# Kernel tuning notes

Measured on AMD Instinct MI355X. Metric: run time of the kernel, lower is better.

Reference implementation:

```python
import jax, jax.numpy as jnp
import numpy as np
import math

IN_DIM = 256
OUT_DIM = 256
MAX_IN = 1024
MAX_OUT = 512
BATCH = 2
SEQ = 1024  # actual_seq_len == max_in_seq here
RED = 2
LN_EPS = 1e-5


def setup_inputs() -> dict:
    key = jax.random.key(0)
    ks = jax.random.split(key, 8)
    N = BATCH * SEQ
    return {
        "x": jax.random.normal(ks[0], (N, IN_DIM), dtype=jnp.float32),
        "M": jax.random.uniform(ks[1], (OUT_DIM, IN_DIM), minval=-0.5, maxval=0.5, dtype=jnp.float32),
        "P": jax.random.uniform(ks[2], (OUT_DIM, OUT_DIM), minval=-0.1, maxval=0.1, dtype=jnp.float32),
        "Linker": jax.random.uniform(ks[3], (MAX_IN, MAX_OUT), minval=-0.1, maxval=0.1, dtype=jnp.float32),
        "ln_gamma": jnp.ones((OUT_DIM,), dtype=jnp.float32),
        "ln_beta": jnp.zeros((OUT_DIM,), dtype=jnp.float32),
        "res_W": jax.random.uniform(ks[4], (OUT_DIM, IN_DIM), minval=-0.1, maxval=0.1, dtype=jnp.float32),
        "res_linker": jax.random.uniform(ks[5], (MAX_IN, MAX_OUT), minval=-0.1, maxval=0.1, dtype=jnp.float32),
        "actual_seq_len": SEQ,
    }


def _layer_norm(z, gamma, beta):
    mu = jnp.mean(z, axis=-1, keepdims=True)
    var = jnp.mean((z - mu) ** 2, axis=-1, keepdims=True)
    return (z - mu) * jax.lax.rsqrt(var + LN_EPS) * gamma + beta


def _periods():
    i = jnp.arange(OUT_DIM, dtype=jnp.float32)[:, None]
    j = jnp.arange(OUT_DIM, dtype=jnp.float32)[None, :]
    return i * OUT_DIM + j + 2.0  # (D, D)


def reference(x, M, P, Linker, ln_gamma, ln_beta, res_W, res_linker, actual_seq_len):
    S = int(actual_seq_len)
    N, _ = x.shape
    B = N // S
    D = OUT_DIM
    out_seq = max(1, S // RED)

    # Z = LN(x @ M^T)
    Z = _layer_norm(x @ M.T, ln_gamma, ln_beta)  # (N, D)

    # position transform: T[k,i] = sum_j Z[k,j] * P[i,j] * cos(2*pi*k / periods[i,j])
    k = jnp.arange(N, dtype=jnp.float32)[:, None, None]  # (N,1,1)
    phi = jnp.cos(2.0 * math.pi * k / _periods()[None])   # (N, D, D)
    T = jnp.einsum('kj,ij,kij->ki', Z, P, phi)            # (N, D)

    # adaptive sequence-length transform via Linker slice
    L = Linker[:S, :out_seq]                               # (S, out_seq)
    U = jnp.einsum('bsd,st->btd', T.reshape(B, S, D), L).reshape(B * out_seq, D)

    # 'separate' residual path
    rfeat = (x @ res_W.T).reshape(B, S, D)
    rL = res_linker[:S, :out_seq]
    residual = jnp.einsum('bsd,st->btd', rfeat, rL).reshape(B * out_seq, D)

    return U + residual
```

## Files before the change

kernel.cpp:

```cpp
#include <hip/hip_runtime.h>

#define D256 256
#define KT 8
#define S_SEQ 1024
#define OUTSEQ 512

typedef __attribute__((ext_vector_type(8))) short bf16x8;
typedef __attribute__((ext_vector_type(8))) unsigned short u16x8;
typedef __attribute__((ext_vector_type(4))) float f32x4;

__device__ inline unsigned short f2bf(float f) {
  unsigned u = __float_as_uint(f);
  return (unsigned short)((u + 0x7fffu + ((u >> 16) & 1u)) >> 16);
}

__global__ __launch_bounds__(256) void k_prep(const float* __restrict__ M,
                                              const float* __restrict__ resW,
                                              const float* __restrict__ P,
                                              const float* __restrict__ Linker,
                                              const float* __restrict__ rLinker,
                                              float2* __restrict__ MW,
                                              float4* __restrict__ PIt4,
                                              unsigned short* __restrict__ LinkTb) {
  __shared__ float tl[64][65];
  const int tid = threadIdx.x;
  if (blockIdx.x < 256) {
    const int j = blockIdx.x;
    const int t = tid;
    MW[j * D256 + t] = make_float2(M[t * D256 + j], resW[t * D256 + j]);
    const float p = (float)(t * D256 + j + 2);
    const float ip = 1.0f / p;
    const float cb2 = 2.0f * __builtin_amdgcn_cosf(ip);
    PIt4[j * D256 + t] = make_float4(P[t * D256 + j], ip, cb2, 0.0f);
    return;
  }
  const int tb = blockIdx.x - 256;
  const int st = tb & 31;
  const int tt = tb >> 5;
  const int s0 = st * 64, t0 = tt * 64;
  const float* src = (s0 < 1024) ? (Linker + (size_t)s0 * OUTSEQ)
                                 : (rLinker + (size_t)(s0 - 1024) * OUTSEQ);
  {
    const int sy = tid >> 2, sx = tid & 3;
    #pragma unroll
    for (int c = 0; c < 4; ++c) {
      const int ci = sx + c * 4;
      const float4 v = *(const float4*)&src[sy * OUTSEQ + t0 + ci * 4];
      tl[ci * 4 + 0][sy] = v.x;
      tl[ci * 4 + 1][sy] = v.y;
      tl[ci * 4 + 2][sy] = v.z;
      tl[ci * 4 + 3][sy] = v.w;
    }
  }
  __syncthreads();
  {
    const int ty = tid >> 2, tx = tid & 3;
    u16x8 o0, o1;
    #pragma unroll
    for (int e = 0; e < 8; ++e) o0[e] = f2bf(tl[ty][tx * 16 + e]);
    #pragma unroll
    for (int e = 0; e < 8; ++e) o1[e] = f2bf(tl[ty][tx * 16 + 8 + e]);
    unsigned short* dst = LinkTb + (size_t)(t0 + ty) * 2048 + s0 + tx * 16;
    *(u16x8*)dst = o0;
    *(u16x8*)(dst + 8) = o1;
  }
}

__global__ __launch_bounds__(1024, 4) void k_AB(const float* __restrict__ x,
                                                const float2* __restrict__ MW,
                                                const float4* __restrict__ PIt4,
                                                const float* __restrict__ gamma,
                                                const float* __restrict__ beta,
                                                unsigned short* __restrict__ Bt) {
  __shared__ float Xs[D256][12];
  __shared__ float red[4][KT][D256];
  __shared__ float mu_s[KT], rs_s[KT];
  const int tid = threadIdx.x;
  const int i = tid & 255;
  const int h = tid >> 8;
  const int j0 = h * 64;
  const int k0 = blockIdx.x * KT;

  Xs[i][h]     = x[(k0 + h) * D256 + i];
  Xs[i][h + 4] = x[(k0 + h + 4) * D256 + i];
  __syncthreads();

  float aM[KT], aR[KT];
  #pragma unroll
  for (int r = 0; r < KT; ++r) { aM[r] = 0.f; aR[r] = 0.f; }
  {
    const float2* mwp = MW + i;
    #pragma unroll 8
    for (int jj = 0; jj < 64; ++jj) {
      const int j = j0 + jj;
      const float2 mw = mwp[j * D256];
      const float4 z0 = *(const float4*)&Xs[j][0];
      const float4 z1 = *(const float4*)&Xs[j][4];
      aM[0] = fmaf(z0.x, mw.x, aM[0]); aR[0] = fmaf(z0.x, mw.y, aR[0]);
      aM[1] = fmaf(z0.y, mw.x, aM[1]); aR[1] = fmaf(z0.y, mw.y, aR[1]);
      aM[2] = fmaf(z0.z, mw.x, aM[2]); aR[2] = fmaf(z0.z, mw.y, aR[2]);
      aM[3] = fmaf(z0.w, mw.x, aM[3]); aR[3] = fmaf(z0.w, mw.y, aR[3]);
      aM[4] = fmaf(z1.x, mw.x, aM[4]); aR[4] = fmaf(z1.x, mw.y, aR[4]);
      aM[5] = fmaf(z1.y, mw.x, aM[5]); aR[5] = fmaf(z1.y, mw.y, aR[5]);
      aM[6] = fmaf(z1.z, mw.x, aM[6]); aR[6] = fmaf(z1.z, mw.y, aR[6]);
      aM[7] = fmaf(z1.w, mw.x, aM[7]); aR[7] = fmaf(z1.w, mw.y, aR[7]);
    }
  }

  #pragma unroll
  for (int r = 0; r < KT; ++r) red[h][r][i] = aR[r];
  __syncthreads();
  if (tid < 256) {
    u16x8 o;
    #pragma unroll
    for (int r = 0; r < KT; ++r)
      o[r] = f2bf(red[0][r][tid] + red[1][r][tid] + red[2][r][tid] + red[3][r][tid]);
    *(u16x8*)(Bt + (size_t)tid * 4096 + 2048 + k0) = o;
  }
  __syncthreads();

  #pragma unroll
  for (int r = 0; r < KT; ++r) red[h][r][i] = aM[r];
  __syncthreads();
  #pragma unroll
  for (int p = 0; p < 2; ++p) {
    const int r = h * 2 + p;
    Xs[i][r] = red[0][r][i] + red[1][r][i] + red[2][r][i] + red[3][r][i];
  }
  __syncthreads();

  const int w = tid >> 6, lane = tid & 63;
  if (w < KT) {
    float s = 0.f, sq = 0.f;
    #pragma unroll
    for (int l = 0; l < 4; ++l) {
      const float v = Xs[lane + 64 * l][w];
      s += v;
      sq = fmaf(v, v, sq);
    }
    #pragma unroll
    for (int off = 32; off; off >>= 1) {
      s += __shfl_down(s, off);
      sq += __shfl_down(sq, off);
    }
    if (lane == 0) {
      const float m = s * (1.0f / 256.0f);
      const float var = sq * (1.0f / 256.0f) - m * m;
      mu_s[w] = m;
      rs_s[w] = rsqrtf(var + 1e-5f);
    }
  }
  __syncthreads();
  {
    const float g = gamma[i], be = beta[i];
    #pragma unroll
    for (int p = 0; p < 2; ++p) {
      const int r = h + 4 * p;
      Xs[i][r] = (Xs[i][r] - mu_s[r]) * rs_s[r] * g + be;
    }
  }
  __syncthreads();

  float accT[KT] = {};
  const float kf0 = (float)k0, kf1 = (float)(k0 + 1);
  {
    const float4* pip = PIt4 + i;
    #pragma unroll 4
    for (int jj = 0; jj < 64; ++jj) {
      const int j = j0 + jj;
      const float4 pi = pip[j * D256];
      const float4 z0 = *(const float4*)&Xs[j][0];
      const float4 z1 = *(const float4*)&Xs[j][4];
      const float r0 = __builtin_amdgcn_fractf(kf0 * pi.y);
      const float r1 = __builtin_amdgcn_fractf(kf1 * pi.y);
      float c0 = __builtin_amdgcn_cosf(r0);
      float c1 = __builtin_amdgcn_cosf(r1);
      accT[0] = fmaf(z0.x * pi.x, c0, accT[0]);
      accT[1] = fmaf(z0.y * pi.x, c1, accT[1]);
      float c2;
      c2 = fmaf(pi.z, c1, -c0); accT[2] = fmaf(z0.z * pi.x, c2, accT[2]); c0 = c1; c1 = c2;
      c2 = fmaf(pi.z, c1, -c0); accT[3] = fmaf(z0.w * pi.x, c2, accT[3]); c0 = c1; c1 = c2;
      c2 = fmaf(pi.z, c1, -c0); accT[4] = fmaf(z1.x * pi.x, c2, accT[4]); c0 = c1; c1 = c2;
      c2 = fmaf(pi.z, c1, -c0); accT[5] = fmaf(z1.y * pi.x, c2, accT[5]); c0 = c1; c1 = c2;
      c2 = fmaf(pi.z, c1, -c0); accT[6] = fmaf(z1.z * pi.x, c2, accT[6]); c0 = c1; c1 = c2;
      c2 = fmaf(pi.z, c1, -c0); accT[7] = fmaf(z1.w * pi.x, c2, accT[7]);
    }
  }
  #pragma unroll
  for (int r = 0; r < KT; ++r) red[h][r][i] = accT[r];
  __syncthreads();
  if (tid < 256) {
    u16x8 o;
    #pragma unroll
    for (int r = 0; r < KT; ++r)
      o[r] = f2bf(red[0][r][tid] + red[1][r][tid] + red[2][r][tid] + red[3][r][tid]);
    *(u16x8*)(Bt + (size_t)tid * 4096 + k0) = o;
  }
}

__global__ __launch_bounds__(256) void k_Cm(const unsigned short* __restrict__ LinkTb,
                                            const unsigned short* __restrict__ Bt,
                                            float* __restrict__ part) {
  const int bid = blockIdx.x;
  const int kc = bid & 7;
  const int dt = (bid >> 3) & 3;
  const int tt = (bid >> 5) & 7;
  const int b  = bid >> 8;
  const int wv = threadIdx.x >> 6;
  const int l  = threadIdx.x & 63;
  const int wm = wv >> 1, wn = wv & 1;
  const int t0 = tt * 64 + wm * 32;
  const int d0 = dt * 64 + wn * 32;
  const int m  = l & 15;
  const int q  = l >> 4;
  const int sc0 = kc * 128;

  f32x4 acc00 = {}, acc01 = {}, acc10 = {}, acc11 = {};
  const unsigned short* Arow = LinkTb + (size_t)(t0 + m) * 2048;
  const unsigned short* Brow = Bt + (size_t)(d0 + m) * 4096;

  #pragma unroll
  for (int seg = 0; seg < 2; ++seg) {
    const int acol = seg * 1024 + sc0 + q * 8;
    const int bcol = seg * 2048 + b * 1024 + sc0 + q * 8;
    #pragma unroll
    for (int ks = 0; ks < 4; ++ks) {
      const bf16x8 a0 = *(const bf16x8*)(Arow + acol + ks * 32);
      const bf16x8 a1 = *(const bf16x8*)(Arow + 16 * 2048 + acol + ks * 32);
      const bf16x8 b0 = *(const bf16x8*)(Brow + bcol + ks * 32);
      const bf16x8 b1 = *(const bf16x8*)(Brow + 16 * 4096 + bcol + ks * 32);
      acc00 = __builtin_amdgcn_mfma_f32_16x16x32_bf16(a0, b0, acc00, 0, 0, 0);
      acc01 = __builtin_amdgcn_mfma_f32_16x16x32_bf16(a0, b1, acc01, 0, 0, 0);
      acc10 = __builtin_amdgcn_mfma_f32_16x16x32_bf16(a1, b0, acc10, 0, 0, 0);
      acc11 = __builtin_amdgcn_mfma_f32_16x16x32_bf16(a1, b1, acc11, 0, 0, 0);
    }
  }

  float* pb = part + ((size_t)kc << 18) + (size_t)(b * 512 + t0 + q * 4) * D256 + d0 + m;
  #pragma unroll
  for (int reg = 0; reg < 4; ++reg) {
    pb[(0 + reg) * D256 + 0]       = acc00[reg];
    pb[(0 + reg) * D256 + 16]      = acc01[reg];
    pb[(16 + reg) * D256 + 0]      = acc10[reg];
    pb[(16 + reg) * D256 + 16]     = acc11[reg];
  }
}

__global__ __launch_bounds__(256) void k_Cred(const float* __restrict__ part,
                                              float* __restrict__ out) {
  const int row = blockIdx.x;
  const int d   = threadIdx.x;
  float s = 0.f;
  #pragma unroll
  for (int kc = 0; kc < 8; ++kc)
    s += part[((size_t)kc << 18) + row * D256 + d];
  out[row * D256 + d] = s;
}

extern "C" void kernel_launch(void* const* d_in, const int* in_sizes, int n_in,
                              void* d_out, int out_size, void* d_ws, size_t ws_size,
                              hipStream_t stream) {
  const float* x       = (const float*)d_in[0];
  const float* M       = (const float*)d_in[1];
  const float* P       = (const float*)d_in[2];
  const float* Linker  = (const float*)d_in[3];
  const float* gamma   = (const float*)d_in[4];
  const float* beta    = (const float*)d_in[5];
  const float* resW    = (const float*)d_in[6];
  const float* rLinker = (const float*)d_in[7];
  float* out = (float*)d_out;

  char* ws = (char*)d_ws;
  float2*         MW     = (float2*)(ws);
  float4*         PIt4   = (float4*)(ws + 512 * 1024);
  unsigned short* LinkTb = (unsigned short*)(ws + 1536 * 1024);
  unsigned short* Bt     = (unsigned short*)(ws + 3584 * 1024);
  float*          part   = (float*)(ws + 5632 * 1024);

  hipLaunchKernelGGL(k_prep, dim3(512),  dim3(256),  0, stream,
                     M, resW, P, Linker, rLinker, MW, PIt4, LinkTb);
  hipLaunchKernelGGL(k_AB,   dim3(256),  dim3(1024), 0, stream,
                     x, MW, PIt4, gamma, beta, Bt);
  hipLaunchKernelGGL(k_Cm,   dim3(512),  dim3(256),  0, stream, LinkTb, Bt, part);
  hipLaunchKernelGGL(k_Cred, dim3(1024), dim3(256),  0, stream, part, out);
}
```

Before: 49.78 us.

## Split fused AB kernel into MFMA GEMM+LayerNorm and separate cosine-transform kernel

The fp32 FMA projection of x by M and res_W inside the fused kernel is replaced by a bf16 MFMA GEMM kernel (k_Azn). Its inputs are converted to bf16 in extra prep blocks, and it writes the normalized Z to global memory in fp32. The cosine position transform moves to its own kernel with twice as many smaller blocks, each handling half the output columns, to raise parallelism. This adds a kernel launch, a global round trip for Z, and bf16 rounding of x and the weights before LayerNorm, which may reduce accuracy.

Result: slower. 52.86 us (+6.2%).

```diff
diff --git a/kernel.cpp b/kernel.cpp
--- a/kernel.cpp
+++ b/kernel.cpp
@@ -14,27 +14,46 @@
   return (unsigned short)((u + 0x7fffu + ((u >> 16) & 1u)) >> 16);
 }
 
-__global__ __launch_bounds__(256) void k_prep(const float* __restrict__ M,
+__global__ __launch_bounds__(256) void k_prep(const float* __restrict__ x,
+                                              const float* __restrict__ M,
                                               const float* __restrict__ resW,
                                               const float* __restrict__ P,
                                               const float* __restrict__ Linker,
                                               const float* __restrict__ rLinker,
-                                              float2* __restrict__ MW,
                                               float4* __restrict__ PIt4,
-                                              unsigned short* __restrict__ LinkTb) {
+                                              unsigned short* __restrict__ LinkTb,
+                                              unsigned short* __restrict__ xb,
+                                              unsigned short* __restrict__ Mb,
+                                              unsigned short* __restrict__ Wb) {
   __shared__ float tl[64][65];
   const int tid = threadIdx.x;
-  if (blockIdx.x < 256) {
-    const int j = blockIdx.x;
+  const int blk = blockIdx.x;
+  if (blk < 256) {
+    const int j = blk;
     const int t = tid;
-    MW[j * D256 + t] = make_float2(M[t * D256 + j], resW[t * D256 + j]);
     const float p = (float)(t * D256 + j + 2);
     const float ip = 1.0f / p;
     const float cb2 = 2.0f * __builtin_amdgcn_cosf(ip);
     PIt4[j * D256 + t] = make_float4(P[t * D256 + j], ip, cb2, 0.0f);
     return;
   }
-  const int tb = blockIdx.x - 256;
+  if (blk >= 512) {
+    const float* src;
+    unsigned short* dst;
+    size_t base;
+    if (blk < 768)      { src = x;    dst = xb; base = (size_t)(blk - 512) * 2048; }
+    else if (blk < 800) { src = M;    dst = Mb; base = (size_t)(blk - 768) * 2048; }
+    else                { src = resW; dst = Wb; base = (size_t)(blk - 800) * 2048; }
+    const size_t off = base + (size_t)tid * 8;
+    const float4 v0 = *(const float4*)(src + off);
+    const float4 v1 = *(const float4*)(src + off + 4);
+    u16x8 o;
+    o[0] = f2bf(v0.x); o[1] = f2bf(v0.y); o[2] = f2bf(v0.z); o[3] = f2bf(v0.w);
+    o[4] = f2bf(v1.x); o[5] = f2bf(v1.y); o[6] = f2bf(v1.z); o[7] = f2bf(v1.w);
+    *(u16x8*)(dst + off) = o;
+    return;
+  }
+  const int tb = blk - 256;
   const int st = tb & 31;
   const int tt = tb >> 5;
   const int s0 = st * 64, t0 = tt * 64;
@@ -66,75 +85,51 @@
   }
 }
 
-__global__ __launch_bounds__(1024, 4) void k_AB(const float* __restrict__ x,
-                                                const float2* __restrict__ MW,
-                                                const float4* __restrict__ PIt4,
-                                                const float* __restrict__ gamma,
-                                                const float* __restrict__ beta,
-                                                unsigned short* __restrict__ Bt) {
-  __shared__ float Xs[D256][12];
-  __shared__ float red[4][KT][D256];
-  __shared__ float mu_s[KT], rs_s[KT];
-  const int tid = threadIdx.x;
-  const int i = tid & 255;
-  const int h = tid >> 8;
-  const int j0 = h * 64;
-  const int k0 = blockIdx.x * KT;
-
-  Xs[i][h]     = x[(k0 + h) * D256 + i];
-  Xs[i][h + 4] = x[(k0 + h + 4) * D256 + i];
-  __syncthreads();
-
-  float aM[KT], aR[KT];
-  #pragma unroll
-  for (int r = 0; r < KT; ++r) { aM[r] = 0.f; aR[r] = 0.f; }
-  {
-    const float2* mwp = MW + i;
-    #pragma unroll 8
-    for (int jj = 0; jj < 64; ++jj) {
-      const int j = j0 + jj;
-      const float2 mw = mwp[j * D256];
-      const float4 z0 = *(const float4*)&Xs[j][0];
-      const float4 z1 = *(const float4*)&Xs[j][4];
-      aM[0] = fmaf(z0.x, mw.x, aM[0]); aR[0] = fmaf(z0.x, mw.y, aR[0]);
-      aM[1] = fmaf(z0.y, mw.x, aM[1]); aR[1] = fmaf(z0.y, mw.y, aR[1]);
-      aM[2] = fmaf(z0.z, mw.x, aM[2]); aR[2] = fmaf(z0.z, mw.y, aR[2]);
-      aM[3] = fmaf(z0.w, mw.x, aM[3]); aR[3] = fmaf(z0.w, mw.y, aR[3]);
-      aM[4] = fmaf(z1.x, mw.x, aM[4]); aR[4] = fmaf(z1.x, mw.y, aR[4]);
-      aM[5] = fmaf(z1.y, mw.x, aM[5]); aR[5] = fmaf(z1.y, mw.y, aR[5]);
-      aM[6] = fmaf(z1.z, mw.x, aM[6]); aR[6] = fmaf(z1.z, mw.y, aR[6]);
-      aM[7] = fmaf(z1.w, mw.x, aM[7]); aR[7] = fmaf(z1.w, mw.y, aR[7]);
-    }
-  }
-
-  #pragma unroll
-  for (int r = 0; r < KT; ++r) red[h][r][i] = aR[r];
-  __syncthreads();
-  if (tid < 256) {
-    u16x8 o;
-    #pragma unroll
-    for (int r = 0; r < KT; ++r)
-      o[r] = f2bf(red[0][r][tid] + red[1][r][tid] + red[2][r][tid] + red[3][r][tid]);
-    *(u16x8*)(Bt + (size_t)tid * 4096 + 2048 + k0) = o;
-  }
-  __syncthreads();
-
-  #pragma unroll
-  for (int r = 0; r < KT; ++r) red[h][r][i] = aM[r];
-  __syncthreads();
-  #pragma unroll
-  for (int p = 0; p < 2; ++p) {
-    const int r = h * 2 + p;
-    Xs[i][r] = red[0][r][i] + red[1][r][i] + red[2][r][i] + red[3][r][i];
-  }
-  __syncthreads();
-
-  const int w = tid >> 6, lane = tid & 63;
-  if (w < KT) {
+__global__ __launch_bounds__(256) void k_Azn(const unsigned short* __restrict__ xb,
+                                             const unsigned short* __restrict__ Mb,
+                                             const unsigned short* __restrict__ Wb,
+                                             const float* __restrict__ gamma,
+                                             const float* __restrict__ beta,
+                                             float* __restrict__ Zb,
+                                             unsigned short* __restrict__ Bt) {
+  __shared__ float Zs[16][D256];
+  __shared__ float Rs[16][D256];
+  __shared__ float mu_s[16], rs_s[16];
+  const int k0 = blockIdx.x * 16;
+  const int w = threadIdx.x >> 6;
+  const int l = threadIdx.x & 63;
+  const int m = l & 15, q = l >> 4;
+
+  f32x4 aZ[4] = {}, aR[4] = {};
+  const unsigned short* Arow = xb + (size_t)(k0 + m) * D256;
+  #pragma unroll
+  for (int ks = 0; ks < 8; ++ks) {
+    const bf16x8 a = *(const bf16x8*)(Arow + ks * 32 + q * 8);
+    #pragma unroll
+    for (int cf = 0; cf < 4; ++cf) {
+      const int o = w * 64 + cf * 16 + m;
+      const bf16x8 bz = *(const bf16x8*)(Mb + (size_t)o * D256 + ks * 32 + q * 8);
+      const bf16x8 br = *(const bf16x8*)(Wb + (size_t)o * D256 + ks * 32 + q * 8);
+      aZ[cf] = __builtin_amdgcn_mfma_f32_16x16x32_bf16(a, bz, aZ[cf], 0, 0, 0);
+      aR[cf] = __builtin_amdgcn_mfma_f32_16x16x32_bf16(a, br, aR[cf], 0, 0, 0);
+    }
+  }
+  #pragma unroll
+  for (int cf = 0; cf < 4; ++cf) {
+    #pragma unroll
+    for (int r = 0; r < 4; ++r) {
+      Zs[q * 4 + r][w * 64 + cf * 16 + m] = aZ[cf][r];
+      Rs[q * 4 + r][w * 64 + cf * 16 + m] = aR[cf][r];
+    }
+  }
+  __syncthreads();
+
+  #pragma unroll
+  for (int rr = w; rr < 16; rr += 4) {
     float s = 0.f, sq = 0.f;
     #pragma unroll
-    for (int l = 0; l < 4; ++l) {
-      const float v = Xs[lane + 64 * l][w];
+    for (int p = 0; p < 4; ++p) {
+      const float v = Zs[rr][l + 64 * p];
       s += v;
       sq = fmaf(v, v, sq);
     }
@@ -143,32 +138,61 @@
       s += __shfl_down(s, off);
       sq += __shfl_down(sq, off);
     }
-    if (lane == 0) {
-      const float m = s * (1.0f / 256.0f);
-      const float var = sq * (1.0f / 256.0f) - m * m;
-      mu_s[w] = m;
-      rs_s[w] = rsqrtf(var + 1e-5f);
-    }
-  }
-  __syncthreads();
-  {
-    const float g = gamma[i], be = beta[i];
-    #pragma unroll
-    for (int p = 0; p < 2; ++p) {
-      const int r = h + 4 * p;
-      Xs[i][r] = (Xs[i][r] - mu_s[r]) * rs_s[r] * g + be;
-    }
+    if (l == 0) {
+      const float mu = s * (1.0f / 256.0f);
+      const float var = sq * (1.0f / 256.0f) - mu * mu;
+      mu_s[rr] = mu;
+      rs_s[rr] = rsqrtf(var + 1e-5f);
+    }
+  }
+  __syncthreads();
+
+  {
+    const int t = threadIdx.x;
+    const float g = gamma[t], be = beta[t];
+    u16x8 o0, o1;
+    #pragma unroll
+    for (int rr = 0; rr < 16; ++rr) {
+      Zb[(size_t)(k0 + rr) * D256 + t] = (Zs[rr][t] - mu_s[rr]) * rs_s[rr] * g + be;
+      const unsigned short rb = f2bf(Rs[rr][t]);
+      if (rr < 8) o0[rr] = rb; else o1[rr - 8] = rb;
+    }
+    unsigned short* dst = Bt + (size_t)t * 4096 + 2048 + k0;
+    *(u16x8*)dst = o0;
+    *(u16x8*)(dst + 8) = o1;
+  }
+}
+
+__global__ __launch_bounds__(512) void k_B(const float* __restrict__ Zb,
+                                           const float4* __restrict__ PIt4,
+                                           unsigned short* __restrict__ Bt) {
+  __shared__ float Xs[D256][12];
+  __shared__ float red[4][KT][128];
+  const int tid = threadIdx.x;
+  const int il = tid & 127;
+  const int jq = tid >> 7;
+  const int kt = blockIdx.x >> 1;
+  const int ih = blockIdx.x & 1;
+  const int k0 = kt * KT;
+  const int ib = ih * 128 + il;
+
+  {
+    const int i = tid & 255;
+    const int h2 = tid >> 8;
+    #pragma unroll
+    for (int r = 0; r < 4; ++r)
+      Xs[i][h2 * 4 + r] = Zb[(size_t)(k0 + h2 * 4 + r) * D256 + i];
   }
   __syncthreads();
 
   float accT[KT] = {};
   const float kf0 = (float)k0, kf1 = (float)(k0 + 1);
   {
-    const float4* pip = PIt4 + i;
+    const float4* pip = PIt4 + ib;
     #pragma unroll 4
     for (int jj = 0; jj < 64; ++jj) {
-      const int j = j0 + jj;
-      const float4 pi = pip[j * D256];
+      const int j = jq * 64 + jj;
+      const float4 pi = pip[(size_t)j * D256];
       const float4 z0 = *(const float4*)&Xs[j][0];
       const float4 z1 = *(const float4*)&Xs[j][4];
       const float r0 = __builtin_amdgcn_fractf(kf0 * pi.y);
@@ -187,14 +211,14 @@
     }
   }
   #pragma unroll
-  for (int r = 0; r < KT; ++r) red[h][r][i] = accT[r];
-  __syncthreads();
-  if (tid < 256) {
+  for (int r = 0; r < KT; ++r) red[jq][r][il] = accT[r];
+  __syncthreads();
+  if (tid < 128) {
     u16x8 o;
     #pragma unroll
     for (int r = 0; r < KT; ++r)
       o[r] = f2bf(red[0][r][tid] + red[1][r][tid] + red[2][r][tid] + red[3][r][tid]);
-    *(u16x8*)(Bt + (size_t)tid * 4096 + k0) = o;
+    *(u16x8*)(Bt + (size_t)(ih * 128 + tid) * 4096 + k0) = o;
   }
 }
 
@@ -239,10 +263,10 @@
   float* pb = part + ((size_t)kc << 18) + (size_t)(b * 512 + t0 + q * 4) * D256 + d0 + m;
   #pragma unroll
   for (int reg = 0; reg < 4; ++reg) {
-    pb[(0 + reg) * D256 + 0]       = acc00[reg];
-    pb[(0 + reg) * D256 + 16]      = acc01[reg];
-    pb[(16 + reg) * D256 + 0]      = acc10[reg];
-    pb[(16 + reg) * D256 + 16]     = acc11[reg];
+    pb[(0 + reg) * D256 + 0]   = acc00[reg];
+    pb[(0 + reg) * D256 + 16]  = acc01[reg];
+    pb[(16 + reg) * D256 + 0]  = acc10[reg];
+    pb[(16 + reg) * D256 + 16] = acc11[reg];
   }
 }
 
@@ -271,16 +295,20 @@
   float* out = (float*)d_out;
 
   char* ws = (char*)d_ws;
-  float2*         MW     = (float2*)(ws);
-  float4*         PIt4   = (float4*)(ws + 512 * 1024);
-  unsigned short* LinkTb = (unsigned short*)(ws + 1536 * 1024);
-  unsigned short* Bt     = (unsigned short*)(ws + 3584 * 1024);
-  float*          part   = (float*)(ws + 5632 * 1024);
-
-  hipLaunchKernelGGL(k_prep, dim3(512),  dim3(256),  0, stream,
-                     M, resW, P, Linker, rLinker, MW, PIt4, LinkTb);
-  hipLaunchKernelGGL(k_AB,   dim3(256),  dim3(1024), 0, stream,
-                     x, MW, PIt4, gamma, beta, Bt);
-  hipLaunchKernelGGL(k_Cm,   dim3(512),  dim3(256),  0, stream, LinkTb, Bt, part);
-  hipLaunchKernelGGL(k_Cred, dim3(1024), dim3(256),  0, stream, part, out);
-}
+  float4*         PIt4   = (float4*)(ws);
+  unsigned short* LinkTb = (unsigned short*)(ws + 1024 * 1024);
+  unsigned short* Bt     = (unsigned short*)(ws + 3072 * 1024);
+  unsigned short* xb     = (unsigned short*)(ws + 5120 * 1024);
+  unsigned short* Mb     = (unsigned short*)(ws + 6144 * 1024);
+  unsigned short* Wb     = (unsigned short*)(ws + 6272 * 1024);
+  float*          Zb     = (float*)(ws + 6400 * 1024);
+  float*          part   = (float*)(ws + 8448 * 1024);
+
+  hipLaunchKernelGGL(k_prep, dim3(832),  dim3(256), 0, stream,
+                     x, M, resW, P, Linker, rLinker, PIt4, LinkTb, xb, Mb, Wb);
+  hipLaunchKernelGGL(k_Azn,  dim3(128),  dim3(256), 0, stream,
+                     xb, Mb, Wb, gamma, beta, Zb, Bt);
+  hipLaunchKernelGGL(k_B,    dim3(512),  dim3(512), 0, stream, Zb, PIt4, Bt);
+  hipLaunchKernelGGL(k_Cm,   dim3(512),  dim3(256), 0, stream, LinkTb, Bt, part);
+  hipLaunchKernelGGL(k_Cred, dim3(1024), dim3(256), 0, stream, part, out);
+}
```
